# Optimization experiments

Measured on AMD Instinct MI355X. Metric: run time of the kernel, lower is better.

Reference implementation:

```python
import jax, jax.numpy as jnp
import numpy as np

DIM = 512
N_HEAD = 4
WIN = (5, 9)

def setup_inputs() -> dict:
    key = jax.random.key(0)
    ks = jax.random.split(key, 9)
    s = DIM ** -0.5
    x = jax.random.normal(ks[0], (1, 8, 60, 108, DIM), jnp.float32)
    Wq = jax.random.normal(ks[1], (DIM, DIM), jnp.float32) * s
    bq = jax.random.normal(ks[2], (DIM,), jnp.float32) * 0.02
    Wk = jax.random.normal(ks[3], (DIM, DIM), jnp.float32) * s
    bk = jax.random.normal(ks[4], (DIM,), jnp.float32) * 0.02
    Wv = jax.random.normal(ks[5], (DIM, DIM), jnp.float32) * s
    bv = jax.random.normal(ks[6], (DIM,), jnp.float32) * 0.02
    Wp = jax.random.normal(ks[7], (DIM, DIM), jnp.float32) * s
    bp = jax.random.normal(ks[8], (DIM,), jnp.float32) * 0.02
    return {"x": x, "Wq": Wq, "bq": bq, "Wk": Wk, "bk": bk,
            "Wv": Wv, "bv": bv, "Wp": Wp, "bp": bp}

def reference(x, Wq, bq, Wk, bk, Wv, bv, Wp, bp):
    b, t, h, w, c = x.shape
    w_h, w_w = WIN
    n_head = N_HEAD
    c_head = c // n_head
    n_wh = -(-h // w_h)
    n_ww = -(-w // w_w)
    new_h, new_w = n_wh * w_h, n_ww * w_w
    pad_b, pad_r = new_h - h, new_w - w
    if pad_b > 0 or pad_r > 0:
        x = jnp.pad(x, ((0, 0), (0, 0), (0, pad_b), (0, pad_r), (0, 0)))
    # torch nn.Linear: y = x @ W.T + b, weight shape (out, in)
    q = jnp.einsum('bthwc,dc->bthwd', x, Wq) + bq
    k = jnp.einsum('bthwc,dc->bthwd', x, Wk) + bk
    v = jnp.einsum('bthwc,dc->bthwd', x, Wv) + bv

    def part(z):
        # (b,t,H,W,c) -> (b, n_windows, n_head, t*w_h*w_w, c_head)
        z = z.reshape(b, t, n_wh, w_h, n_ww, w_w, n_head, c_head)
        z = z.transpose(0, 2, 4, 6, 1, 3, 5, 7)
        return z.reshape(b, n_wh * n_ww, n_head, t * w_h * w_w, c_head)

    qw, kw, vw = part(q), part(k), part(v)
    scale = c_head ** -0.5
    # all (batch, window) attentions batched into one einsum (fused form of the torch double loop)
    scores = jnp.einsum('bwnsc,bwnkc->bwnsk', qw, kw) * scale
    attn = jax.nn.softmax(scores, axis=-1)
    out = jnp.einsum('bwnsk,bwnkc->bwnsc', attn, vw)
    # merge windows back: (b,t,new_h,new_w,c)
    out = out.reshape(b, n_wh, n_ww, n_head, t, w_h, w_w, c_head)
    out = out.transpose(0, 4, 1, 5, 2, 6, 3, 7).reshape(b, t, new_h, new_w, c)
    out = out[:, :, :h, :w, :]
    out = jnp.einsum('bthwc,dc->bthwd', out, Wp) + bp
    return out
```

## Files before the change

kernel.cpp:

```cpp
#include <hip/hip_runtime.h>

typedef _Float16 f16;
typedef _Float16 f16x8 __attribute__((ext_vector_type(8)));
typedef _Float16 f16x4 __attribute__((ext_vector_type(4)));
typedef float f32x4 __attribute__((ext_vector_type(4)));
typedef unsigned int u32;
typedef unsigned int u32x4 __attribute__((ext_vector_type(4)));

#define MFMA16(a, b, c) __builtin_amdgcn_mfma_f32_16x16x32_f16(a, b, c, 0, 0, 0)

__device__ __forceinline__ void async_copy16(f16* lds, const f16* g) {
    __builtin_amdgcn_global_load_lds(
        (const __attribute__((address_space(1))) unsigned int*)g,
        (__attribute__((address_space(3))) unsigned int*)lds,
        16, 0, 0);
}

__global__ __launch_bounds__(256) void prep_convert(
    const float* __restrict__ x, f16* __restrict__ xh,
    const float* __restrict__ Wq, const float* __restrict__ Wk,
    const float* __restrict__ Wv, const float* __restrict__ Wp,
    const float* __restrict__ bq, const float* __restrict__ bk,
    const float* __restrict__ bv,
    f16* __restrict__ Wqkv, f16* __restrict__ Wph, float* __restrict__ bqkv,
    int* __restrict__ tokmap)
{
    if (blockIdx.x < 12960) {
        int i = blockIdx.x * 256 + threadIdx.x;
        f32x4 a = *(const f32x4*)(x + (size_t)i * 8);
        f32x4 b = *(const f32x4*)(x + (size_t)i * 8 + 4);
        f16x8 h = { (f16)a[0], (f16)a[1], (f16)a[2], (f16)a[3],
                    (f16)b[0], (f16)b[1], (f16)b[2], (f16)b[3] };
        *(f16x8*)(xh + (size_t)i * 8) = h;
        return;
    }
    int i = (blockIdx.x - 12960) * 256 + threadIdx.x;
    if (i < 786432) {
        int r = i >> 9, c = i & 511;
        const float* src = (r < 512) ? Wq : (r < 1024) ? Wk : Wv;
        Wqkv[i] = (f16)src[(r & 511) * 512 + c];
    } else if (i < 786432 + 262144) {
        int j = i - 786432;
        Wph[j] = (f16)Wp[j];
    } else if (i < 786432 + 262144 + 1536) {
        int j = i - (786432 + 262144);
        bqkv[j] = (j < 512) ? bq[j] : (j < 1024) ? bk[j - 512] : bv[j - 1024];
    } else if (i < 786432 + 262144 + 1536 + 51840) {
        int j = i - (786432 + 262144 + 1536);
        int t_ = j / 6480, rem = j % 6480;
        int hh = rem / 108, ww = rem % 108;
        int win = (hh / 5) * 12 + (ww / 9);
        int s = t_ * 45 + (hh % 5) * 9 + (ww % 9);
        tokmap[j] = win * 1440 + s;
    }
}

__global__ __launch_bounds__(256, 3) void qkv_gemm(
    const f16* __restrict__ Xh, const f16* __restrict__ W,
    const float* __restrict__ bias, const int* __restrict__ tokmap,
    f16* __restrict__ Qp, f16* __restrict__ Kp, f16* __restrict__ Vp)
{
    __shared__ __align__(16) f16 As[3][128 * 32];
    __shared__ __align__(16) f16 Bs[3][128 * 32];
    const int tid = threadIdx.x;
    const int lane = tid & 63, wid = tid >> 6;
    const int g = lane >> 4, l15 = lane & 15;
    const int wr = wid >> 1, wc = wid & 1;

    const int orig = blockIdx.x;
    const int xcd = orig & 7;
    const int wg = (xcd < 4 ? xcd * 608 : 2432 + (xcd - 4) * 607) + (orig >> 3);
    const int bn = wg % 12;
    const int brow = (wg / 12) * 128;

    const f16* Abase = Xh + (size_t)brow * 512;
    const f16* Bbase = W + (size_t)bn * 128 * 512;

    f32x4 acc[4][4] = {};

    #define QKV_STAGE(buf, step)                                              \
        {                                                                     \
            const int k0_ = (step) * 32;                                      \
            _Pragma("unroll")                                                 \
            for (int rr = 0; rr < 2; ++rr) {                                  \
                int idx = rr * 256 + tid;                                     \
                int row = idx >> 2, ch = idx & 3;                             \
                int sch = ch ^ ((row >> 1) & 3);                              \
                async_copy16(&As[buf][idx * 8],                               \
                             Abase + (size_t)row * 512 + k0_ + sch * 8);      \
                async_copy16(&Bs[buf][idx * 8],                               \
                             Bbase + (size_t)row * 512 + k0_ + sch * 8);      \
            }                                                                 \
        }

    QKV_STAGE(0, 0);
    QKV_STAGE(1, 1);

    int cur = 0;
    for (int t = 0; t < 16; ++t) {
        if (t < 15) asm volatile("s_waitcnt vmcnt(4)" ::: "memory");
        else        asm volatile("s_waitcnt vmcnt(0)" ::: "memory");
        __builtin_amdgcn_s_barrier();
        __builtin_amdgcn_sched_barrier(0);
        if (t + 2 < 16) {
            int stg = cur + 2; if (stg >= 3) stg -= 3;
            QKV_STAGE(stg, t + 2);
        }
        f16x8 a[4], b[4];
        #pragma unroll
        for (int m = 0; m < 4; ++m) {
            int arow = wr * 64 + m * 16 + l15;
            int sl = g ^ ((arow >> 1) & 3);
            a[m] = *(const f16x8*)&As[cur][arow * 32 + sl * 8];
        }
        #pragma unroll
        for (int n = 0; n < 4; ++n) {
            int brw = wc * 64 + n * 16 + l15;
            int sl = g ^ ((brw >> 1) & 3);
            b[n] = *(const f16x8*)&Bs[cur][brw * 32 + sl * 8];
        }
        __builtin_amdgcn_s_setprio(1);
        #pragma unroll
        for (int m = 0; m < 4; ++m)
            #pragma unroll
            for (int n = 0; n < 4; ++n)
                acc[m][n] = MFMA16(a[m], b[n], acc[m][n]);
        __builtin_amdgcn_s_setprio(0);
        __builtin_amdgcn_s_barrier();
        cur = (cur == 2) ? 0 : cur + 1;
    }
    #undef QKV_STAGE

    const int which = bn >> 2, head = bn & 3;
    f16* dst = (which == 0) ? Qp : (which == 1) ? Kp : Vp;
    #pragma unroll
    for (int m = 0; m < 4; ++m) {
        #pragma unroll
        for (int j = 0; j < 4; ++j) {
            int gm = brow + wr * 64 + m * 16 + g * 4 + j;
            size_t obase = ((size_t)(tokmap[gm] + head * 360)) * 128;
            #pragma unroll
            for (int n = 0; n < 4; ++n) {
                int cidx = wc * 64 + n * 16 + l15;
                float v = acc[m][n][j] + bias[bn * 128 + cidx];
                dst[obase + cidx] = (f16)v;
            }
        }
    }
}

__global__ __launch_bounds__(256, 2) void attn_kernel(
    const f16* __restrict__ Qp, const f16* __restrict__ Kp,
    const f16* __restrict__ Vp, f16* __restrict__ AO)
{
    __shared__ __align__(16) f16 Kl[64 * 140];
    __shared__ __align__(16) f16 Vt[128 * 76];
    __shared__ __align__(16) f16 Pl[192 * 76];

    const int tid = threadIdx.x;
    const int lane = tid & 63, wid = tid >> 6;
    const int g = lane >> 4, l15 = lane & 15;
    const int wh = blockIdx.x >> 1;
    const int half = blockIdx.x & 1;
    const int win = wh >> 2, head = wh & 3;
    const int base = wh * 46080;
    const int qbase = half * 192 + wid * 48;

    const float SC2 = 0.08838834764831845f * 1.4426950408889634f;

    f16x8 qf[3][4];
    #pragma unroll
    for (int qi = 0; qi < 3; ++qi)
        #pragma unroll
        for (int c4 = 0; c4 < 4; ++c4)
            qf[qi][c4] = *(const f16x8*)(Qp + base + (qbase + qi * 16 + l15) * 128 + c4 * 32 + g * 8);

    f32x4 o[3][8] = {};
    float m_r[3] = { -1e30f, -1e30f, -1e30f };
    float l_r[3] = { 0.f, 0.f, 0.f };

    for (int kt = 0; kt < 6; ++kt) {
        #pragma unroll
        for (int it = 0; it < 4; ++it) {
            int idx = it * 256 + tid;
            int krow = idx >> 4, seg = idx & 15;
            f16x8 kv = *(const f16x8*)(Kp + base + (kt * 64 + krow) * 128 + seg * 8);
            *(f16x8*)&Kl[krow * 140 + seg * 8] = kv;
        }
        #pragma unroll
        for (int it = 0; it < 2; ++it) {
            int i2 = it * 256 + tid;
            int kb = i2 >> 6;
            int chp = (i2 & 63) * 2;
            const u32* Vb = (const u32*)(Vp + base);
            u32 d[8];
            #pragma unroll
            for (int i = 0; i < 8; ++i) {
                int kg = kt * 64 + kb * 8 + i;
                d[i] = (kg < 360) ? Vb[kg * 64 + (chp >> 1)] : 0u;
            }
            u32x4 lo, hi;
            #pragma unroll
            for (int jj = 0; jj < 4; ++jj) {
                lo[jj] = (d[2 * jj] & 0xffffu) | (d[2 * jj + 1] << 16);
                hi[jj] = (d[2 * jj] >> 16) | (d[2 * jj + 1] & 0xffff0000u);
            }
            *(u32x4*)&Vt[chp * 76 + kb * 8] = lo;
            *(u32x4*)&Vt[(chp + 1) * 76 + kb * 8] = hi;
        }
        __syncthreads();

        f32x4 sc[4][3] = {};
        __builtin_amdgcn_s_setprio(1);
        #pragma unroll
        for (int c4 = 0; c4 < 4; ++c4) {
            f16x8 ka[4];
            #pragma unroll
            for (int kf = 0; kf < 4; ++kf)
                ka[kf] = *(const f16x8*)&Kl[(kf * 16 + l15) * 140 + c4 * 32 + g * 8];
            #pragma unroll
            for (int kf = 0; kf < 4; ++kf)
                #pragma unroll
                for (int qi = 0; qi < 3; ++qi)
                    sc[kf][qi] = MFMA16(ka[kf], qf[qi][c4], sc[kf][qi]);
        }
        __builtin_amdgcn_s_setprio(0);
        if (kt == 5) {
            #pragma unroll
            for (int kf = 0; kf < 4; ++kf)
                #pragma unroll
                for (int j = 0; j < 4; ++j)
                    if (320 + kf * 16 + g * 4 + j >= 360) {
                        #pragma unroll
                        for (int qi = 0; qi < 3; ++qi) sc[kf][qi][j] = -1e30f;
                    }
        }

        #pragma unroll
        for (int qi = 0; qi < 3; ++qi) {
            float mx = -1e30f;
            #pragma unroll
            for (int kf = 0; kf < 4; ++kf)
                #pragma unroll
                for (int j = 0; j < 4; ++j)
                    mx = fmaxf(mx, sc[kf][qi][j]);
            mx = fmaxf(mx, __shfl_xor(mx, 16));
            mx = fmaxf(mx, __shfl_xor(mx, 32));
            if (!__all(mx - m_r[qi] <= 8.0f)) {
                float mnew = fmaxf(m_r[qi], mx);
                float r = exp2f((m_r[qi] - mnew) * SC2);
                m_r[qi] = mnew;
                l_r[qi] *= r;
                #pragma unroll
                for (int j = 0; j < 4; ++j) {
                    float rj = __shfl(r, g * 4 + j);
                    #pragma unroll
                    for (int chf = 0; chf < 8; ++chf)
                        o[qi][chf][j] *= rj;
                }
            }
            float psum = 0.f;
            #pragma unroll
            for (int kf = 0; kf < 4; ++kf) {
                f16x4 pv;
                #pragma unroll
                for (int j = 0; j < 4; ++j) {
                    float p = exp2f((sc[kf][qi][j] - m_r[qi]) * SC2);
                    psum += p;
                    pv[j] = (f16)p;
                }
                *(f16x4*)&Pl[(wid * 48 + qi * 16 + l15) * 76 + kf * 16 + g * 4] = pv;
            }
            psum += __shfl_xor(psum, 16);
            psum += __shfl_xor(psum, 32);
            l_r[qi] += psum;
        }

        __builtin_amdgcn_s_setprio(1);
        #pragma unroll
        for (int kc = 0; kc < 2; ++kc) {
            f16x8 pa[3], vb[8];
            #pragma unroll
            for (int qi = 0; qi < 3; ++qi)
                pa[qi] = *(const f16x8*)&Pl[(wid * 48 + qi * 16 + l15) * 76 + kc * 32 + g * 8];
            #pragma unroll
            for (int chf = 0; chf < 8; ++chf)
                vb[chf] = *(const f16x8*)&Vt[(chf * 16 + l15) * 76 + kc * 32 + g * 8];
            #pragma unroll
            for (int qi = 0; qi < 3; ++qi)
                #pragma unroll
                for (int chf = 0; chf < 8; ++chf)
                    o[qi][chf] = MFMA16(pa[qi], vb[chf], o[qi][chf]);
        }
        __builtin_amdgcn_s_setprio(0);
        __syncthreads();
    }

    #pragma unroll
    for (int qi = 0; qi < 3; ++qi) {
        #pragma unroll
        for (int j = 0; j < 4; ++j) {
            float lj = __shfl(l_r[qi], g * 4 + j);
            float inv = 1.0f / lj;
            int s = qbase + qi * 16 + g * 4 + j;
            if (s < 360) {
                int t_ = s / 45, s45 = s % 45;
                int hh = (win / 12) * 5 + s45 / 9;
                int ww = (win % 12) * 9 + s45 % 9;
                int mm = t_ * 6480 + hh * 108 + ww;
                #pragma unroll
                for (int chf = 0; chf < 8; ++chf) {
                    int col = head * 128 + chf * 16 + l15;
                    AO[(size_t)mm * 512 + col] = (f16)(o[qi][chf][j] * inv);
                }
            }
        }
    }
}

__global__ __launch_bounds__(256, 3) void proj_gemm(
    const f16* __restrict__ A, const f16* __restrict__ W,
    const float* __restrict__ bias, float* __restrict__ out)
{
    __shared__ __align__(16) f16 As[3][128 * 32];
    __shared__ __align__(16) f16 Bs[3][128 * 32];
    const int tid = threadIdx.x;
    const int lane = tid & 63, wid = tid >> 6;
    const int g = lane >> 4, l15 = lane & 15;
    const int wr = wid >> 1, wc = wid & 1;

    const int orig = blockIdx.x;
    const int xcd = orig & 7;
    const int wg = (xcd < 4 ? xcd * 203 : 812 + (xcd - 4) * 202) + (orig >> 3);
    const int bcol = (wg & 3) * 128;
    const int brow = (wg >> 2) * 128;

    const f16* Abase = A + (size_t)brow * 512;
    const f16* Bbase = W + (size_t)bcol * 512;

    f32x4 acc[4][4] = {};

    #define PROJ_STAGE(buf, step)                                             \
        {                                                                     \
            const int k0_ = (step) * 32;                                      \
            _Pragma("unroll")                                                 \
            for (int rr = 0; rr < 2; ++rr) {                                  \
                int idx = rr * 256 + tid;                                     \
                int row = idx >> 2, ch = idx & 3;                             \
                int sch = ch ^ ((row >> 1) & 3);                              \
                async_copy16(&As[buf][idx * 8],                               \
                             Abase + (size_t)row * 512 + k0_ + sch * 8);      \
                async_copy16(&Bs[buf][idx * 8],                               \
                             Bbase + (size_t)row * 512 + k0_ + sch * 8);      \
            }                                                                 \
        }

    PROJ_STAGE(0, 0);
    PROJ_STAGE(1, 1);

    int cur = 0;
    for (int t = 0; t < 16; ++t) {
        if (t < 15) asm volatile("s_waitcnt vmcnt(4)" ::: "memory");
        else        asm volatile("s_waitcnt vmcnt(0)" ::: "memory");
        __builtin_amdgcn_s_barrier();
        __builtin_amdgcn_sched_barrier(0);
        if (t + 2 < 16) {
            int stg = cur + 2; if (stg >= 3) stg -= 3;
            PROJ_STAGE(stg, t + 2);
        }
        f16x8 a[4], b[4];
        #pragma unroll
        for (int m = 0; m < 4; ++m) {
            int arow = wr * 64 + m * 16 + l15;
            int sl = g ^ ((arow >> 1) & 3);
            a[m] = *(const f16x8*)&As[cur][arow * 32 + sl * 8];
        }
        #pragma unroll
        for (int n = 0; n < 4; ++n) {
            int brw = wc * 64 + n * 16 + l15;
            int sl = g ^ ((brw >> 1) & 3);
            b[n] = *(const f16x8*)&Bs[cur][brw * 32 + sl * 8];
        }
        __builtin_amdgcn_s_setprio(1);
        #pragma unroll
        for (int m = 0; m < 4; ++m)
            #pragma unroll
            for (int n = 0; n < 4; ++n)
                acc[m][n] = MFMA16(a[m], b[n], acc[m][n]);
        __builtin_amdgcn_s_setprio(0);
        __builtin_amdgcn_s_barrier();
        cur = (cur == 2) ? 0 : cur + 1;
    }
    #undef PROJ_STAGE

    #pragma unroll
    for (int m = 0; m < 4; ++m)
        #pragma unroll
        for (int j = 0; j < 4; ++j) {
            int gm = brow + wr * 64 + m * 16 + g * 4 + j;
            #pragma unroll
            for (int n = 0; n < 4; ++n) {
                int gn = bcol + wc * 64 + n * 16 + l15;
                out[(size_t)gm * 512 + gn] = acc[m][n][j] + bias[gn];
            }
        }
}

extern "C" void kernel_launch(void* const* d_in, const int* in_sizes, int n_in,
                              void* d_out, int out_size, void* d_ws, size_t ws_size,
                              hipStream_t stream)
{
    (void)in_sizes; (void)n_in; (void)out_size; (void)ws_size;
    const float* x  = (const float*)d_in[0];
    const float* Wq = (const float*)d_in[1];
    const float* bq = (const float*)d_in[2];
    const float* Wk = (const float*)d_in[3];
    const float* bk = (const float*)d_in[4];
    const float* Wv = (const float*)d_in[5];
    const float* bv = (const float*)d_in[6];
    const float* Wp = (const float*)d_in[7];
    const float* bp = (const float*)d_in[8];

    f16* Qp   = (f16*)d_ws;
    f16* Kp   = Qp + 26542080;
    f16* Vp   = Kp + 26542080;
    f16* AO   = Vp + 26542080;
    f16* xh   = AO;
    f16* Wqkv = AO + 26542080;
    f16* Wph  = Wqkv + 786432;
    float* bqkv = (float*)(Wph + 262144);
    int* tokmap = (int*)(bqkv + 1536);

    prep_convert<<<17265, 256, 0, stream>>>(x, xh, Wq, Wk, Wv, Wp, bq, bk, bv,
                                            Wqkv, Wph, bqkv, tokmap);
    qkv_gemm<<<4860, 256, 0, stream>>>(xh, Wqkv, bqkv, tokmap, Qp, Kp, Vp);
    attn_kernel<<<1152, 256, 0, stream>>>(Qp, Kp, Vp, AO);
    proj_gemm<<<1620, 256, 0, stream>>>(AO, Wph, bp, (float*)d_out);
}
```

Measured before the change: 285.1 us.

## Restructure QKV GEMM into 256x256 tiles with 8-wave interleaved pipeline

```diff
diff --git a/kernel.cpp b/kernel.cpp
--- a/kernel.cpp
+++ b/kernel.cpp
@@ -55,95 +55,143 @@
     }
 }
 
-__global__ __launch_bounds__(256, 3) void qkv_gemm(
+__global__ __launch_bounds__(512, 2) void qkv_gemm(
     const f16* __restrict__ Xh, const f16* __restrict__ W,
     const float* __restrict__ bias, const int* __restrict__ tokmap,
     f16* __restrict__ Qp, f16* __restrict__ Kp, f16* __restrict__ Vp)
 {
-    __shared__ __align__(16) f16 As[3][128 * 32];
-    __shared__ __align__(16) f16 Bs[3][128 * 32];
+    __shared__ __align__(16) f16 As[2][2][128 * 64];
+    __shared__ __align__(16) f16 Bs[2][2][128 * 64];
     const int tid = threadIdx.x;
-    const int lane = tid & 63, wid = tid >> 6;
+    const int lane = tid & 63;
+    const int wid = tid >> 6;
     const int g = lane >> 4, l15 = lane & 15;
-    const int wr = wid >> 1, wc = wid & 1;
+    const int wr = wid >> 2;
+    const int wc = wid & 3;
 
     const int orig = blockIdx.x;
     const int xcd = orig & 7;
-    const int wg = (xcd < 4 ? xcd * 608 : 2432 + (xcd - 4) * 607) + (orig >> 3);
-    const int bn = wg % 12;
-    const int brow = (wg / 12) * 128;
-
-    const f16* Abase = Xh + (size_t)brow * 512;
-    const f16* Bbase = W + (size_t)bn * 128 * 512;
-
-    f32x4 acc[4][4] = {};
-
-    #define QKV_STAGE(buf, step)                                              \
-        {                                                                     \
-            const int k0_ = (step) * 32;                                      \
-            _Pragma("unroll")                                                 \
-            for (int rr = 0; rr < 2; ++rr) {                                  \
-                int idx = rr * 256 + tid;                                     \
-                int row = idx >> 2, ch = idx & 3;                             \
-                int sch = ch ^ ((row >> 1) & 3);                              \
-                async_copy16(&As[buf][idx * 8],                               \
-                             Abase + (size_t)row * 512 + k0_ + sch * 8);      \
-                async_copy16(&Bs[buf][idx * 8],                               \
-                             Bbase + (size_t)row * 512 + k0_ + sch * 8);      \
-            }                                                                 \
-        }
-
-    QKV_STAGE(0, 0);
-    QKV_STAGE(1, 1);
-
-    int cur = 0;
-    for (int t = 0; t < 16; ++t) {
-        if (t < 15) asm volatile("s_waitcnt vmcnt(4)" ::: "memory");
-        else        asm volatile("s_waitcnt vmcnt(0)" ::: "memory");
-        __builtin_amdgcn_s_barrier();
+    const int wg = (xcd < 2 ? xcd * 153 : 306 + (xcd - 2) * 152) + (orig >> 3);
+    const int bn = wg % 6;
+    const int brow = (wg / 6) * 256;
+
+    const f16* Ab = Xh + (size_t)brow * 512;
+    const f16* Bb = W + (size_t)bn * 256 * 512;
+
+    auto stage = [&](int which, int h, int T) {
+        const f16* src = which ? Bb : Ab;
+        f16* dst = which ? &Bs[T & 1][h][0] : &As[T & 1][h][0];
+        #pragma unroll
+        for (int it = 0; it < 2; ++it) {
+            int idx = it * 512 + tid;
+            int row = idx >> 3, sl = idx & 7;
+            int ss = sl ^ (row & 7);
+            async_copy16(dst + idx * 8,
+                         src + (size_t)(h * 128 + row) * 512 + T * 64 + ss * 8);
+        }
+    };
+
+    f32x4 acc[8][4] = {};
+
+    stage(1, 0, 0); stage(1, 1, 0); stage(0, 0, 0); stage(0, 1, 0);
+    stage(1, 0, 1); stage(1, 1, 1);
+    asm volatile("s_waitcnt vmcnt(4)" ::: "memory");
+    __builtin_amdgcn_s_barrier();
+
+    for (int t = 0; t < 8; ++t) {
+        const int p = t & 1;
+        f16x8 a0[8], a1[8], bk0[4], bk1[4];
+
+        #pragma unroll
+        for (int m = 0; m < 8; ++m) {
+            int row = m * 16 + l15;
+            int ss = g ^ (row & 7);
+            a0[m] = *(const f16x8*)&As[p][wr][row * 64 + ss * 8];
+        }
+        #pragma unroll
+        for (int n = 0; n < 4; ++n) {
+            int row = (wc & 1) * 64 + n * 16 + l15;
+            int ss = g ^ (row & 7);
+            bk0[n] = *(const f16x8*)&Bs[p][wc >> 1][row * 64 + ss * 8];
+        }
+        if (t + 1 < 8) stage(0, 0, t + 1);
+        asm volatile("s_waitcnt lgkmcnt(0)" ::: "memory");
         __builtin_amdgcn_sched_barrier(0);
-        if (t + 2 < 16) {
-            int stg = cur + 2; if (stg >= 3) stg -= 3;
-            QKV_STAGE(stg, t + 2);
-        }
-        f16x8 a[4], b[4];
-        #pragma unroll
-        for (int m = 0; m < 4; ++m) {
-            int arow = wr * 64 + m * 16 + l15;
-            int sl = g ^ ((arow >> 1) & 3);
-            a[m] = *(const f16x8*)&As[cur][arow * 32 + sl * 8];
-        }
+        __builtin_amdgcn_s_setprio(1);
+        #pragma unroll
+        for (int m = 0; m < 4; ++m)
+            #pragma unroll
+            for (int n = 0; n < 4; ++n)
+                acc[m][n] = MFMA16(a0[m], bk0[n], acc[m][n]);
+        __builtin_amdgcn_s_setprio(0);
+        __builtin_amdgcn_s_barrier();
+
         #pragma unroll
         for (int n = 0; n < 4; ++n) {
-            int brw = wc * 64 + n * 16 + l15;
-            int sl = g ^ ((brw >> 1) & 3);
-            b[n] = *(const f16x8*)&Bs[cur][brw * 32 + sl * 8];
-        }
+            int row = (wc & 1) * 64 + n * 16 + l15;
+            int ss = (4 + g) ^ (row & 7);
+            bk1[n] = *(const f16x8*)&Bs[p][wc >> 1][row * 64 + ss * 8];
+        }
+        if (t + 1 < 8) stage(0, 1, t + 1);
+        asm volatile("s_waitcnt lgkmcnt(0)" ::: "memory");
+        __builtin_amdgcn_sched_barrier(0);
+        __builtin_amdgcn_s_setprio(1);
+        #pragma unroll
+        for (int m = 4; m < 8; ++m)
+            #pragma unroll
+            for (int n = 0; n < 4; ++n)
+                acc[m][n] = MFMA16(a0[m], bk0[n], acc[m][n]);
+        __builtin_amdgcn_s_setprio(0);
+        __builtin_amdgcn_s_barrier();
+
+        #pragma unroll
+        for (int m = 0; m < 8; ++m) {
+            int row = m * 16 + l15;
+            int ss = (4 + g) ^ (row & 7);
+            a1[m] = *(const f16x8*)&As[p][wr][row * 64 + ss * 8];
+        }
+        if (t + 2 < 8) stage(1, 0, t + 2);
+        asm volatile("s_waitcnt lgkmcnt(0)" ::: "memory");
+        __builtin_amdgcn_sched_barrier(0);
         __builtin_amdgcn_s_setprio(1);
         #pragma unroll
         for (int m = 0; m < 4; ++m)
             #pragma unroll
             for (int n = 0; n < 4; ++n)
-                acc[m][n] = MFMA16(a[m], b[n], acc[m][n]);
-        __builtin_amdgcn_s_setprio(0);
-        __builtin_amdgcn_s_barrier();
-        cur = (cur == 2) ? 0 : cur + 1;
-    }
-    #undef QKV_STAGE
-
-    const int which = bn >> 2, head = bn & 3;
+                acc[m][n] = MFMA16(a1[m], bk1[n], acc[m][n]);
+        __builtin_amdgcn_s_setprio(0);
+        __builtin_amdgcn_s_barrier();
+
+        if (t + 2 < 8) stage(1, 1, t + 2);
+        __builtin_amdgcn_s_setprio(1);
+        #pragma unroll
+        for (int m = 4; m < 8; ++m)
+            #pragma unroll
+            for (int n = 0; n < 4; ++n)
+                acc[m][n] = MFMA16(a1[m], bk1[n], acc[m][n]);
+        __builtin_amdgcn_s_setprio(0);
+        if (t < 6)       asm volatile("s_waitcnt vmcnt(4)" ::: "memory");
+        else if (t == 6) asm volatile("s_waitcnt vmcnt(0)" ::: "memory");
+        __builtin_amdgcn_s_barrier();
+    }
+
+    const int gc0 = bn * 256 + wc * 64;
+    const int which = gc0 >> 9;
+    const int head = (gc0 >> 7) & 3;
     f16* dst = (which == 0) ? Qp : (which == 1) ? Kp : Vp;
     #pragma unroll
-    for (int m = 0; m < 4; ++m) {
+    for (int m = 0; m < 8; ++m) {
         #pragma unroll
         for (int j = 0; j < 4; ++j) {
-            int gm = brow + wr * 64 + m * 16 + g * 4 + j;
-            size_t obase = ((size_t)(tokmap[gm] + head * 360)) * 128;
-            #pragma unroll
-            for (int n = 0; n < 4; ++n) {
-                int cidx = wc * 64 + n * 16 + l15;
-                float v = acc[m][n][j] + bias[bn * 128 + cidx];
-                dst[obase + cidx] = (f16)v;
+            int gm = brow + wr * 128 + m * 16 + g * 4 + j;
+            if (gm < 51840) {
+                size_t obase = ((size_t)(tokmap[gm] + head * 360)) * 128;
+                #pragma unroll
+                for (int n = 0; n < 4; ++n) {
+                    int gcol = gc0 + n * 16 + l15;
+                    float v = acc[m][n][j] + bias[gcol];
+                    dst[obase + (gcol & 127)] = (f16)v;
+                }
             }
         }
     }
@@ -433,7 +481,7 @@
 
     prep_convert<<<17265, 256, 0, stream>>>(x, xh, Wq, Wk, Wv, Wp, bq, bk, bv,
                                             Wqkv, Wph, bqkv, tokmap);
-    qkv_gemm<<<4860, 256, 0, stream>>>(xh, Wqkv, bqkv, tokmap, Qp, Kp, Vp);
+    qkv_gemm<<<1218, 512, 0, stream>>>(xh, Wqkv, bqkv, tokmap, Qp, Kp, Vp);
     attn_kernel<<<1152, 256, 0, stream>>>(Qp, Kp, Vp, AO);
     proj_gemm<<<1620, 256, 0, stream>>>(AO, Wph, bp, (float*)d_out);
 }
```

Result: no change. 289.8 us (+1.7%).
